# Performance work log

Hardware: AMD Instinct MI355X
Metric: run time of the kernel (lower is better)

## Reference

```python
import jax, jax.numpy as jnp
import numpy as np

X = 2048      # hidden units per layer
Z = 4         # number of hidden layers
IN = 512      # input_dim
OUT = 256     # output_dim
B = 64        # batch
T = 128       # time steps
KEEP = 0.7    # Bernoulli keep prob y
RES = [0, 0, 1, 2]  # residual_in (first two unused by the branch structure)
NFUN = 5      # number of candidate transfer functions


def setup_inputs() -> dict:
    key = jax.random.key(0)
    ks = jax.random.split(key, 12)
    f32 = jnp.float32
    x = jax.random.normal(ks[0], (B, T, IN), f32)
    W_in = jax.random.normal(ks[1], (X, IN), f32) * jax.random.bernoulli(ks[2], KEEP, (X, IN)).astype(f32)
    b_in = jax.random.normal(ks[3], (X,), f32)
    W_h = jax.random.normal(ks[4], (Z, X, 2 * X), f32)
    # lateral inhibition block: hidden layer 1, second-half columns, zero diagonal
    lat = jax.random.normal(ks[5], (X, X), f32) * (1.0 - jnp.eye(X, dtype=f32))
    W_h = W_h.at[1, :, X:].set(lat)
    W_h = W_h * jax.random.bernoulli(ks[6], KEEP, (Z, X, 2 * X)).astype(f32)
    b_h = jax.random.normal(ks[7], (Z, X), f32)
    W_out = jax.random.normal(ks[8], (OUT, X), f32) * jax.random.bernoulli(ks[9], KEEP, (OUT, X)).astype(f32)
    b_out = jax.random.normal(ks[10], (OUT,), f32)
    act_ids = jax.random.randint(ks[11], (Z + 1, X), 0, NFUN)
    out_act_ids = jax.random.randint(jax.random.fold_in(key, 99), (OUT,), 0, NFUN)
    return dict(x=x, W_in=W_in, b_in=b_in, W_h=W_h, b_h=b_h,
                W_out=W_out, b_out=b_out, act_ids=act_ids, out_act_ids=out_act_ids)


def _rand_act(h, ids):
    # per-column random nonlinearity: ids [D] in {relu, sigmoid, tanh, leaky_relu(0.1), selu}
    stk = jnp.stack([
        jax.nn.relu(h),
        jax.nn.sigmoid(h),
        jnp.tanh(h),
        jnp.where(h >= 0, h, 0.1 * h),
        jax.nn.selu(h),
    ], axis=0)  # [5, B, D]
    oh = jax.nn.one_hot(ids, NFUN, dtype=h.dtype)  # [D, 5]
    return jnp.einsum('fbd,df->bd', stk, oh)


def _l2norm(v, eps=1e-12):
    # torch F.normalize along dim=1
    return v / jnp.maximum(jnp.linalg.norm(v, axis=1, keepdims=True), eps)


def reference(x, W_in, b_in, W_h, b_h, W_out, b_out, act_ids, out_act_ids):
    batch = x.shape[0]

    def step(carry, xt):
        bp, li = carry  # backprojection state, lateral inhibition state
        h0 = _rand_act(xt @ W_in.T + b_in, act_ids[0])
        h1 = _rand_act(jnp.concatenate([h0, bp], axis=-1) @ W_h[0].T + b_h[0], act_ids[1])
        h2 = _rand_act(jnp.concatenate([h1, li], axis=-1) @ W_h[1].T + b_h[1], act_ids[2])
        li_new = _l2norm(h2)
        outs = [h0, h1, h2]
        for i in range(2, Z):
            hin = jnp.concatenate([outs[i], outs[RES[i]]], axis=-1)
            outs.append(_rand_act(hin @ W_h[i].T + b_h[i], act_ids[i + 1]))
        bp_new = _l2norm(outs[-1])
        yt = _rand_act(outs[-1] @ W_out.T + b_out, out_act_ids)
        return (bp_new, li_new), yt

    init = (jnp.zeros((batch, X), x.dtype), jnp.zeros((batch, X), x.dtype))
    _, ys = jax.lax.scan(step, init, jnp.swapaxes(x, 0, 1))  # scan over time
    return jnp.swapaxes(ys, 0, 1)  # [B, T, OUT]
```

## Files before the change

### kernel.cpp

```cpp
#include <hip/hip_runtime.h>
#include <stdint.h>


typedef __bf16 bf16;
typedef __attribute__((ext_vector_type(8))) __bf16 bf16x8;
typedef __attribute__((ext_vector_type(4))) float f32x4;

#define BATCH 64
#define TSTEPS 128
#define INDIM 512
#define XDIM 2048
#define OUTDIM 256
#define NWG 256
#define SLOTE ((size_t)BATCH * XDIM)

__device__ __forceinline__ float apply_act(float h, int id) {
  switch (id) {
    case 0: return fmaxf(h, 0.0f);
    case 1: return 1.0f / (1.0f + __expf(-h));
    case 2: return tanhf(h);
    case 3: return h >= 0.0f ? h : 0.1f * h;
    default: {
      const float sc = 1.0507009873554805f;
      const float al = 1.6732632423543772f;
      return h > 0.0f ? sc * h : sc * al * (__expf(h) - 1.0f);
    }
  }
}

__device__ __forceinline__ bf16x8 load_n(const bf16* p) {
  return *(const bf16x8*)p;
}
__device__ __forceinline__ bf16x8 load_c(const bf16* p) {
  union { unsigned long long q[2]; bf16x8 v; } u;
  u.q[0] = __hip_atomic_load((const unsigned long long*)p, __ATOMIC_RELAXED,
                             __HIP_MEMORY_SCOPE_AGENT);
  u.q[1] = __hip_atomic_load((const unsigned long long*)p + 1, __ATOMIC_RELAXED,
                             __HIP_MEMORY_SCOPE_AGENT);
  return u.v;
}

__device__ __forceinline__ void gbar(uint32_t* bar, int wg, uint32_t bt) {
  asm volatile("s_waitcnt vmcnt(0)" ::: "memory");
  __syncthreads();
  if (threadIdx.x == 0) {
    const int g = wg >> 5;
    uint32_t* grp = bar + g * 32;
    uint32_t* root = bar + 8 * 32;
    uint32_t* eps = bar + 9 * 32 + g * 32;
    uint32_t prev = __hip_atomic_fetch_add(grp, 1u, __ATOMIC_RELAXED,
                                           __HIP_MEMORY_SCOPE_AGENT);
    if (prev == 32u * bt - 1u) {
      uint32_t pr = __hip_atomic_fetch_add(root, 1u, __ATOMIC_RELAXED,
                                           __HIP_MEMORY_SCOPE_AGENT);
      if (pr == 8u * bt - 1u) {
        for (int i = 0; i < 8; i++)
          __hip_atomic_store(bar + 9 * 32 + i * 32, bt, __ATOMIC_RELAXED,
                             __HIP_MEMORY_SCOPE_AGENT);
        goto done;
      }
    }
    while (__hip_atomic_load(eps, __ATOMIC_RELAXED, __HIP_MEMORY_SCOPE_AGENT) < bt)
      __builtin_amdgcn_s_sleep(2);
  done:;
  }
  __syncthreads();
}

template <bool ALL_COH, bool SCALE_A2, bool EMIT_SS>
__device__ __forceinline__ void phase(
    int nblk, int mrow,
    const bf16* __restrict__ A1, const bf16* __restrict__ A2,
    const bf16* __restrict__ W, const float* __restrict__ bias,
    const int* __restrict__ acts, const float* __restrict__ ss_in,
    float* __restrict__ ss_out, bf16* __restrict__ outb,
    float red[8][16][33]) {
  const int tid = threadIdx.x;
  const int lane = tid & 63;
  const int w = tid >> 6;
  const int l15 = lane & 15;
  const int kb8 = (lane >> 4) * 8;

  const bf16* As = (w >= 4) ? A2 : A1;
  const int koff = (w & 3) * 512;
  const int wk = w * 512;

  const bf16* ap = As + (size_t)(mrow + l15) * 2048 + koff + kb8;
  const bf16* bp0 = W + (size_t)(nblk + l15) * 4096 + wk + kb8;
  const bf16* bp1 = bp0 + (size_t)16 * 4096;

  f32x4 acc0 = {0.f, 0.f, 0.f, 0.f};
  f32x4 acc1 = {0.f, 0.f, 0.f, 0.f};
  if (ALL_COH || w >= 4) {
#pragma unroll
    for (int k = 0; k < 512; k += 32) {
      bf16x8 a = load_c(ap + k);
      bf16x8 b0 = load_n(bp0 + k);
      bf16x8 b1 = load_n(bp1 + k);
      acc0 = __builtin_amdgcn_mfma_f32_16x16x32_bf16(a, b0, acc0, 0, 0, 0);
      acc1 = __builtin_amdgcn_mfma_f32_16x16x32_bf16(a, b1, acc1, 0, 0, 0);
    }
  } else {
#pragma unroll
    for (int k = 0; k < 512; k += 32) {
      bf16x8 a = load_n(ap + k);
      bf16x8 b0 = load_n(bp0 + k);
      bf16x8 b1 = load_n(bp1 + k);
      acc0 = __builtin_amdgcn_mfma_f32_16x16x32_bf16(a, b0, acc0, 0, 0, 0);
      acc1 = __builtin_amdgcn_mfma_f32_16x16x32_bf16(a, b1, acc1, 0, 0, 0);
    }
  }

  const int q4 = lane >> 4;
#pragma unroll
  for (int r = 0; r < 4; r++) red[w][q4 * 4 + r][l15] = acc0[r];
#pragma unroll
  for (int r = 0; r < 4; r++) red[w][q4 * 4 + r][16 + l15] = acc1[r];
  __syncthreads();

  if (tid < 256) {
    const int row = tid >> 4;
    const int c0 = (tid & 15) * 2;
    const int rg = mrow + row;

    float scale = 1.0f;
    if (SCALE_A2) {
      float ssv = __hip_atomic_load(ss_in + rg, __ATOMIC_RELAXED,
                                    __HIP_MEMORY_SCOPE_AGENT);
      scale = 1.0f / fmaxf(sqrtf(ssv), 1e-12f);
    }

    float v[2];
#pragma unroll
    for (int j = 0; j < 2; j++) {
      int c = c0 + j;
      float lo = red[0][row][c] + red[1][row][c] + red[2][row][c] + red[3][row][c];
      float hi = red[4][row][c] + red[5][row][c] + red[6][row][c] + red[7][row][c];
      float pre = (SCALE_A2 ? (lo + scale * hi) : (lo + hi)) + bias[nblk + c];
      v[j] = apply_act(pre, acts[nblk + c]);
    }
    if (EMIT_SS) {
      float ss = v[0] * v[0] + v[1] * v[1];
      ss += __shfl_xor(ss, 1);
      ss += __shfl_xor(ss, 2);
      ss += __shfl_xor(ss, 4);
      ss += __shfl_xor(ss, 8);
      if ((tid & 15) == 0) atomicAdd(ss_out + rg, ss);
    }
    union { bf16 b2[2]; uint32_t u; } pk;
    pk.b2[0] = (bf16)v[0];
    pk.b2[1] = (bf16)v[1];
    __hip_atomic_store((uint32_t*)(outb + (size_t)rg * 2048 + nblk + c0), pk.u,
                       __ATOMIC_RELAXED, __HIP_MEMORY_SCOPE_AGENT);
  }
}

struct Params {
  const bf16* h0;
  bf16* h0m;
  const bf16* whb;
  const float* b_h;
  const int* act_ids;
  bf16 *h1, *h2a, *h2b, *h3, *extra;
  float *ss_li, *ss_bp;
  uint32_t* bar;
};

__global__ __launch_bounds__(512, 2) void bnn_persistent(Params p) {
  __shared__ float red[8][16][33];
  const int wg = blockIdx.x;
  const int nblk = (wg & 63) * 32;
  const int mrow = (wg >> 6) * 16;
  const size_t wstr = (size_t)XDIM * 2 * XDIM;
  uint32_t bt = 0;

  for (int t = 0; t < TSTEPS; t++) {
    const bf16* h0t = p.h0 + (size_t)t * SLOTE;
    const bf16* slotA = (t < 2) ? (p.extra + (size_t)t * SLOTE)
                                : (p.h0 + (size_t)(t - 2) * SLOTE);
    bf16* slotD = (t + 1 < 2) ? (p.extra + (size_t)(t + 1) * SLOTE)
                              : (p.h0m + (size_t)(t - 1) * SLOTE);
    bf16* h2n = (t & 1) ? p.h2b : p.h2a;
    bf16* h2o = (t & 1) ? p.h2a : p.h2b;

    phase<false, true, false>(nblk, mrow, h0t, slotA, p.whb, p.b_h,
                              p.act_ids + XDIM, p.ss_bp + t * BATCH, nullptr,
                              p.h1, red);
    gbar(p.bar, wg, ++bt);
    phase<true, true, true>(nblk, mrow, p.h1, h2o, p.whb + wstr, p.b_h + XDIM,
                            p.act_ids + 2 * XDIM, p.ss_li + t * BATCH,
                            p.ss_li + (t + 1) * BATCH, h2n, red);
    gbar(p.bar, wg, ++bt);
    phase<true, false, false>(nblk, mrow, h2n, p.h1, p.whb + 2 * wstr,
                              p.b_h + 2 * XDIM, p.act_ids + 3 * XDIM, nullptr,
                              nullptr, p.h3, red);
    gbar(p.bar, wg, ++bt);
    phase<true, false, true>(nblk, mrow, p.h3, h2n, p.whb + 3 * wstr,
                             p.b_h + 3 * XDIM, p.act_ids + 4 * XDIM, nullptr,
                             p.ss_bp + (t + 1) * BATCH, slotD, red);
    gbar(p.bar, wg, ++bt);
  }
}

__global__ __launch_bounds__(256) void h0_gemm(
    const bf16* __restrict__ A, const bf16* __restrict__ W,
    const float* __restrict__ bias, const int* __restrict__ acts,
    bf16* __restrict__ outp) {
  const int tid = threadIdx.x;
  const int lane = tid & 63;
  const int wv = tid >> 6;
  const int wm = (wv & 1) * 32;
  const int wn = (wv >> 1) * 64;
  const int nblk = blockIdx.x * 128;
  const int mblk = blockIdx.y * 64;
  const int l15 = lane & 15;
  const int kb8 = (lane >> 4) * 8;

  f32x4 acc[2][4];
  const f32x4 zero = {0.f, 0.f, 0.f, 0.f};
#pragma unroll
  for (int i = 0; i < 2; i++)
#pragma unroll
    for (int j = 0; j < 4; j++) acc[i][j] = zero;

  for (int kt = 0; kt < INDIM; kt += 32) {
    bf16x8 a[2], b[4];
#pragma unroll
    for (int mt = 0; mt < 2; mt++) {
      int m = mblk + wm + mt * 16 + l15;
      a[mt] = *(const bf16x8*)(A + (size_t)m * INDIM + kt + kb8);
    }
#pragma unroll
    for (int nt = 0; nt < 4; nt++) {
      int n = nblk + wn + nt * 16 + l15;
      b[nt] = *(const bf16x8*)(W + (size_t)n * INDIM + kt + kb8);
    }
#pragma unroll
    for (int mt = 0; mt < 2; mt++)
#pragma unroll
      for (int nt = 0; nt < 4; nt++)
        acc[mt][nt] = __builtin_amdgcn_mfma_f32_16x16x32_bf16(a[mt], b[nt], acc[mt][nt], 0, 0, 0);
  }

#pragma unroll
  for (int mt = 0; mt < 2; mt++) {
#pragma unroll
    for (int nt = 0; nt < 4; nt++) {
      int n = nblk + wn + nt * 16 + l15;
      float bv = bias[n];
      int aid = acts[n];
#pragma unroll
      for (int rr = 0; rr < 4; rr++) {
        int m = wm + mt * 16 + (lane >> 4) * 4 + rr;
        float v = apply_act(acc[mt][nt][rr] + bv, aid);
        int rowg = mblk + m;
        int bb = rowg >> 7;
        int tt = rowg & 127;
        outp[((size_t)tt * BATCH + bb) * XDIM + n] = (bf16)v;
      }
    }
  }
}

__global__ __launch_bounds__(256) void ybat_gemm(
    const bf16* __restrict__ extra, const bf16* __restrict__ h0,
    const bf16* __restrict__ Wout, const float* __restrict__ bout,
    const int* __restrict__ oact, float* __restrict__ out) {
  const int t = blockIdx.y;
  const int s = t + 1;
  const bf16* A = (s < 2) ? (extra + (size_t)s * SLOTE)
                          : (h0 + (size_t)(s - 2) * SLOTE);
  const int tid = threadIdx.x;
  const int lane = tid & 63;
  const int wv = tid >> 6;
  const int wm = (wv & 1) * 32;
  const int wn = (wv >> 1) * 64;
  const int nblk = blockIdx.x * 128;
  const int l15 = lane & 15;
  const int kb8 = (lane >> 4) * 8;

  f32x4 acc[2][4];
  const f32x4 zero = {0.f, 0.f, 0.f, 0.f};
#pragma unroll
  for (int i = 0; i < 2; i++)
#pragma unroll
    for (int j = 0; j < 4; j++) acc[i][j] = zero;

  for (int kt = 0; kt < XDIM; kt += 32) {
    bf16x8 a[2], b[4];
#pragma unroll
    for (int mt = 0; mt < 2; mt++) {
      int m = wm + mt * 16 + l15;
      a[mt] = *(const bf16x8*)(A + (size_t)m * XDIM + kt + kb8);
    }
#pragma unroll
    for (int nt = 0; nt < 4; nt++) {
      int n = nblk + wn + nt * 16 + l15;
      b[nt] = *(const bf16x8*)(Wout + (size_t)n * XDIM + kt + kb8);
    }
#pragma unroll
    for (int mt = 0; mt < 2; mt++)
#pragma unroll
      for (int nt = 0; nt < 4; nt++)
        acc[mt][nt] = __builtin_amdgcn_mfma_f32_16x16x32_bf16(a[mt], b[nt], acc[mt][nt], 0, 0, 0);
  }

#pragma unroll
  for (int mt = 0; mt < 2; mt++) {
#pragma unroll
    for (int nt = 0; nt < 4; nt++) {
      int n = nblk + wn + nt * 16 + l15;
      float bv = bout[n];
      int aid = oact[n];
#pragma unroll
      for (int rr = 0; rr < 4; rr++) {
        int b = wm + mt * 16 + (lane >> 4) * 4 + rr;
        float v = apply_act(acc[mt][nt][rr] + bv, aid);
        out[((size_t)b * TSTEPS + t) * OUTDIM + n] = v;
      }
    }
  }
}

__global__ __launch_bounds__(256) void cvt_bf16(
    const float* __restrict__ in, bf16* __restrict__ out, int n4) {
  int i = blockIdx.x * 256 + threadIdx.x;
  if (i < n4) {
    float4 v = ((const float4*)in)[i];
    union { bf16 b[4]; unsigned long long u; } pk;
    pk.b[0] = (bf16)v.x;
    pk.b[1] = (bf16)v.y;
    pk.b[2] = (bf16)v.z;
    pk.b[3] = (bf16)v.w;
    ((unsigned long long*)out)[i] = pk.u;
  }
}

__global__ __launch_bounds__(256) void zero32(uint32_t* __restrict__ p, int n) {
  int i = blockIdx.x * 256 + threadIdx.x;
  if (i < n) p[i] = 0u;
}

extern "C" void kernel_launch(void* const* d_in, const int* in_sizes, int n_in,
                              void* d_out, int out_size, void* d_ws, size_t ws_size,
                              hipStream_t stream) {
  const float* x     = (const float*)d_in[0];
  const float* W_in  = (const float*)d_in[1];
  const float* b_in  = (const float*)d_in[2];
  const float* W_h   = (const float*)d_in[3];
  const float* b_h   = (const float*)d_in[4];
  const float* W_out = (const float*)d_in[5];
  const float* b_out = (const float*)d_in[6];
  const int* act_ids = (const int*)d_in[7];
  const int* out_act = (const int*)d_in[8];
  float* out = (float*)d_out;

  char* w = (char*)d_ws;
  bf16* xbf   = (bf16*)w; w += (size_t)BATCH * TSTEPS * INDIM * 2;
  bf16* winb  = (bf16*)w; w += (size_t)XDIM * INDIM * 2;
  bf16* whb   = (bf16*)w; w += (size_t)4 * XDIM * (2 * XDIM) * 2;
  bf16* woutb = (bf16*)w; w += (size_t)OUTDIM * XDIM * 2;
  bf16* h0    = (bf16*)w; w += (size_t)TSTEPS * SLOTE * 2;
  bf16* h1    = (bf16*)w; w += SLOTE * 2;
  bf16* h3    = (bf16*)w; w += SLOTE * 2;
  char* zstart = w;
  bf16* extra = (bf16*)w; w += 2 * SLOTE * 2;
  bf16* h2a   = (bf16*)w; w += SLOTE * 2;
  bf16* h2b   = (bf16*)w; w += SLOTE * 2;
  float* ss_li = (float*)w; w += (size_t)(TSTEPS + 1) * BATCH * 4;
  float* ss_bp = (float*)w; w += (size_t)(TSTEPS + 1) * BATCH * 4;
  uint32_t* bar = (uint32_t*)w; w += 17 * 32 * 4;
  int zero_u32 = (int)((w - zstart) / 4);

  cvt_bf16<<<4096, 256, 0, stream>>>(x, xbf, (BATCH * TSTEPS * INDIM) / 4);
  cvt_bf16<<<1024, 256, 0, stream>>>(W_in, winb, (XDIM * INDIM) / 4);
  cvt_bf16<<<32768, 256, 0, stream>>>(W_h, whb, (4 * XDIM * 2 * XDIM) / 4);
  cvt_bf16<<<512, 256, 0, stream>>>(W_out, woutb, (OUTDIM * XDIM) / 4);
  zero32<<<(zero_u32 + 255) / 256, 256, 0, stream>>>((uint32_t*)zstart, zero_u32);
  h0_gemm<<<dim3(16, 128), 256, 0, stream>>>(xbf, winb, b_in, act_ids, h0);

  Params P;
  P.h0 = h0; P.h0m = h0; P.whb = whb; P.b_h = b_h; P.act_ids = act_ids;
  P.h1 = h1; P.h2a = h2a; P.h2b = h2b; P.h3 = h3; P.extra = extra;
  P.ss_li = ss_li; P.ss_bp = ss_bp; P.bar = bar;

  void* kargs[] = {&P};
  hipLaunchCooperativeKernel((const void*)bnn_persistent, dim3(NWG), dim3(512),
                             kargs, 0, stream);

  ybat_gemm<<<dim3(2, TSTEPS), 256, 0, stream>>>(
      extra, h0, woutb, b_out, out_act, out);
}
```

Measured before the change: 10.47 ms.

## Stage activation rows in LDS and retile persistent GEMM to 8x64 blocks

```diff
diff --git a/kernel.cpp b/kernel.cpp
--- a/kernel.cpp
+++ b/kernel.cpp
@@ -5,6 +5,7 @@
 typedef __bf16 bf16;
 typedef __attribute__((ext_vector_type(8))) __bf16 bf16x8;
 typedef __attribute__((ext_vector_type(4))) float f32x4;
+typedef __attribute__((ext_vector_type(4))) int i32x4;
 
 #define BATCH 64
 #define TSTEPS 128
@@ -13,6 +14,7 @@
 #define OUTDIM 256
 #define NWG 256
 #define SLOTE ((size_t)BATCH * XDIM)
+#define LDSROW 4104
 
 __device__ __forceinline__ float apply_act(float h, int id) {
   switch (id) {
@@ -26,18 +28,6 @@
       return h > 0.0f ? sc * h : sc * al * (__expf(h) - 1.0f);
     }
   }
-}
-
-__device__ __forceinline__ bf16x8 load_n(const bf16* p) {
-  return *(const bf16x8*)p;
-}
-__device__ __forceinline__ bf16x8 load_c(const bf16* p) {
-  union { unsigned long long q[2]; bf16x8 v; } u;
-  u.q[0] = __hip_atomic_load((const unsigned long long*)p, __ATOMIC_RELAXED,
-                             __HIP_MEMORY_SCOPE_AGENT);
-  u.q[1] = __hip_atomic_load((const unsigned long long*)p + 1, __ATOMIC_RELAXED,
-                             __HIP_MEMORY_SCOPE_AGENT);
-  return u.v;
 }
 
 __device__ __forceinline__ void gbar(uint32_t* bar, int wg, uint32_t bt) {
@@ -67,60 +57,81 @@
   __syncthreads();
 }
 
-template <bool ALL_COH, bool SCALE_A2, bool EMIT_SS>
+template <bool A1_CACHED, bool SCALE_A2, bool EMIT_SS>
 __device__ __forceinline__ void phase(
-    int nblk, int mrow,
-    const bf16* __restrict__ A1, const bf16* __restrict__ A2,
-    const bf16* __restrict__ W, const float* __restrict__ bias,
-    const int* __restrict__ acts, const float* __restrict__ ss_in,
-    float* __restrict__ ss_out, bf16* __restrict__ outb,
-    float red[8][16][33]) {
+    int nblk, int mrow, const bf16* __restrict__ A1,
+    const bf16* __restrict__ A2, const bf16* __restrict__ W,
+    const float* __restrict__ bias, const int* __restrict__ acts,
+    const float* __restrict__ ss_in, float* __restrict__ ss_out,
+    bf16* __restrict__ outb, bf16* sA, float red[8][8][66]) {
   const int tid = threadIdx.x;
   const int lane = tid & 63;
   const int w = tid >> 6;
   const int l15 = lane & 15;
-  const int kb8 = (lane >> 4) * 8;
-
-  const bf16* As = (w >= 4) ? A2 : A1;
-  const int koff = (w & 3) * 512;
+  const int q4 = lane >> 4;
+  const int kb8 = q4 * 8;
+
+  {
+    const bf16* base = (tid < 256) ? (A1 + (size_t)tid * 8)
+                                   : (A2 + (size_t)(tid - 256) * 8);
+#pragma unroll
+    for (int b = 0; b < 2; b++) {
+      i32x4 t0, t1, t2, t3;
+      const bf16* s0 = base + (size_t)(mrow + b * 4 + 0) * 2048;
+      const bf16* s1 = base + (size_t)(mrow + b * 4 + 1) * 2048;
+      const bf16* s2 = base + (size_t)(mrow + b * 4 + 2) * 2048;
+      const bf16* s3 = base + (size_t)(mrow + b * 4 + 3) * 2048;
+      if (A1_CACHED && tid < 256) {
+        t0 = *(const i32x4*)s0; t1 = *(const i32x4*)s1;
+        t2 = *(const i32x4*)s2; t3 = *(const i32x4*)s3;
+      } else {
+        asm volatile(
+            "global_load_dwordx4 %0, %4, off sc0 sc1\n\t"
+            "global_load_dwordx4 %1, %5, off sc0 sc1\n\t"
+            "global_load_dwordx4 %2, %6, off sc0 sc1\n\t"
+            "global_load_dwordx4 %3, %7, off sc0 sc1\n\t"
+            "s_waitcnt vmcnt(0)"
+            : "=&v"(t0), "=&v"(t1), "=&v"(t2), "=&v"(t3)
+            : "v"(s0), "v"(s1), "v"(s2), "v"(s3)
+            : "memory");
+      }
+      bf16* d = sA + (size_t)tid * 8 + (size_t)(b * 4) * LDSROW;
+      *(i32x4*)(d + 0 * LDSROW) = t0;
+      *(i32x4*)(d + 1 * LDSROW) = t1;
+      *(i32x4*)(d + 2 * LDSROW) = t2;
+      *(i32x4*)(d + 3 * LDSROW) = t3;
+    }
+  }
+  __syncthreads();
+
   const int wk = w * 512;
-
-  const bf16* ap = As + (size_t)(mrow + l15) * 2048 + koff + kb8;
-  const bf16* bp0 = W + (size_t)(nblk + l15) * 4096 + wk + kb8;
-  const bf16* bp1 = bp0 + (size_t)16 * 4096;
-
+  const bf16* lam = sA + (size_t)(l15 & 7) * LDSROW + wk + kb8;
+  const bf16* bw = W + (size_t)(nblk + l15) * 4096 + wk + kb8;
   f32x4 acc0 = {0.f, 0.f, 0.f, 0.f};
-  f32x4 acc1 = {0.f, 0.f, 0.f, 0.f};
-  if (ALL_COH || w >= 4) {
-#pragma unroll
-    for (int k = 0; k < 512; k += 32) {
-      bf16x8 a = load_c(ap + k);
-      bf16x8 b0 = load_n(bp0 + k);
-      bf16x8 b1 = load_n(bp1 + k);
-      acc0 = __builtin_amdgcn_mfma_f32_16x16x32_bf16(a, b0, acc0, 0, 0, 0);
-      acc1 = __builtin_amdgcn_mfma_f32_16x16x32_bf16(a, b1, acc1, 0, 0, 0);
-    }
-  } else {
-#pragma unroll
-    for (int k = 0; k < 512; k += 32) {
-      bf16x8 a = load_n(ap + k);
-      bf16x8 b0 = load_n(bp0 + k);
-      bf16x8 b1 = load_n(bp1 + k);
-      acc0 = __builtin_amdgcn_mfma_f32_16x16x32_bf16(a, b0, acc0, 0, 0, 0);
-      acc1 = __builtin_amdgcn_mfma_f32_16x16x32_bf16(a, b1, acc1, 0, 0, 0);
-    }
-  }
-
-  const int q4 = lane >> 4;
-#pragma unroll
-  for (int r = 0; r < 4; r++) red[w][q4 * 4 + r][l15] = acc0[r];
-#pragma unroll
-  for (int r = 0; r < 4; r++) red[w][q4 * 4 + r][16 + l15] = acc1[r];
+  f32x4 acc1 = acc0, acc2 = acc0, acc3 = acc0;
+#pragma unroll
+  for (int kk = 0; kk < 512; kk += 32) {
+    bf16x8 a = *(const bf16x8*)(lam + kk);
+    acc0 = __builtin_amdgcn_mfma_f32_16x16x32_bf16(a, *(const bf16x8*)(bw + kk), acc0, 0, 0, 0);
+    acc1 = __builtin_amdgcn_mfma_f32_16x16x32_bf16(a, *(const bf16x8*)(bw + (size_t)16 * 4096 + kk), acc1, 0, 0, 0);
+    acc2 = __builtin_amdgcn_mfma_f32_16x16x32_bf16(a, *(const bf16x8*)(bw + (size_t)32 * 4096 + kk), acc2, 0, 0, 0);
+    acc3 = __builtin_amdgcn_mfma_f32_16x16x32_bf16(a, *(const bf16x8*)(bw + (size_t)48 * 4096 + kk), acc3, 0, 0, 0);
+  }
+
+  if (q4 < 2) {
+#pragma unroll
+    for (int r = 0; r < 4; r++) {
+      red[w][q4 * 4 + r][0 * 16 + l15] = acc0[r];
+      red[w][q4 * 4 + r][1 * 16 + l15] = acc1[r];
+      red[w][q4 * 4 + r][2 * 16 + l15] = acc2[r];
+      red[w][q4 * 4 + r][3 * 16 + l15] = acc3[r];
+    }
+  }
   __syncthreads();
 
   if (tid < 256) {
-    const int row = tid >> 4;
-    const int c0 = (tid & 15) * 2;
+    const int row = tid >> 5;
+    const int c0 = (tid & 31) * 2;
     const int rg = mrow + row;
 
     float scale = 1.0f;
@@ -145,7 +156,8 @@
       ss += __shfl_xor(ss, 2);
       ss += __shfl_xor(ss, 4);
       ss += __shfl_xor(ss, 8);
-      if ((tid & 15) == 0) atomicAdd(ss_out + rg, ss);
+      ss += __shfl_xor(ss, 16);
+      if ((tid & 31) == 0) atomicAdd(ss_out + rg, ss);
     }
     union { bf16 b2[2]; uint32_t u; } pk;
     pk.b2[0] = (bf16)v[0];
@@ -167,10 +179,11 @@
 };
 
 __global__ __launch_bounds__(512, 2) void bnn_persistent(Params p) {
-  __shared__ float red[8][16][33];
+  __shared__ bf16 sA[8 * LDSROW];
+  __shared__ float red[8][8][66];
   const int wg = blockIdx.x;
-  const int nblk = (wg & 63) * 32;
-  const int mrow = (wg >> 6) * 16;
+  const int nblk = (wg & 31) * 64;
+  const int mrow = (wg >> 5) * 8;
   const size_t wstr = (size_t)XDIM * 2 * XDIM;
   uint32_t bt = 0;
 
@@ -183,21 +196,21 @@
     bf16* h2n = (t & 1) ? p.h2b : p.h2a;
     bf16* h2o = (t & 1) ? p.h2a : p.h2b;
 
-    phase<false, true, false>(nblk, mrow, h0t, slotA, p.whb, p.b_h,
-                              p.act_ids + XDIM, p.ss_bp + t * BATCH, nullptr,
-                              p.h1, red);
+    phase<true, true, false>(nblk, mrow, h0t, slotA, p.whb, p.b_h,
+                             p.act_ids + XDIM, p.ss_bp + t * BATCH, nullptr,
+                             p.h1, sA, red);
     gbar(p.bar, wg, ++bt);
-    phase<true, true, true>(nblk, mrow, p.h1, h2o, p.whb + wstr, p.b_h + XDIM,
-                            p.act_ids + 2 * XDIM, p.ss_li + t * BATCH,
-                            p.ss_li + (t + 1) * BATCH, h2n, red);
+    phase<false, true, true>(nblk, mrow, p.h1, h2o, p.whb + wstr, p.b_h + XDIM,
+                             p.act_ids + 2 * XDIM, p.ss_li + t * BATCH,
+                             p.ss_li + (t + 1) * BATCH, h2n, sA, red);
     gbar(p.bar, wg, ++bt);
-    phase<true, false, false>(nblk, mrow, h2n, p.h1, p.whb + 2 * wstr,
-                              p.b_h + 2 * XDIM, p.act_ids + 3 * XDIM, nullptr,
-                              nullptr, p.h3, red);
+    phase<false, false, false>(nblk, mrow, h2n, p.h1, p.whb + 2 * wstr,
+                               p.b_h + 2 * XDIM, p.act_ids + 3 * XDIM, nullptr,
+                               nullptr, p.h3, sA, red);
     gbar(p.bar, wg, ++bt);
-    phase<true, false, true>(nblk, mrow, p.h3, h2n, p.whb + 3 * wstr,
-                             p.b_h + 3 * XDIM, p.act_ids + 4 * XDIM, nullptr,
-                             p.ss_bp + (t + 1) * BATCH, slotD, red);
+    phase<false, false, true>(nblk, mrow, p.h3, h2n, p.whb + 3 * wstr,
+                              p.b_h + 3 * XDIM, p.act_ids + 4 * XDIM, nullptr,
+                              p.ss_bp + (t + 1) * BATCH, slotD, sA, red);
     gbar(p.bar, wg, ++bt);
   }
 }
```

New measurement: 16.81 ms. +60.6%, slower.
